# Optimization experiments

Measured on AMD Instinct MI355X. Metric: run time of the kernel, lower is better.

Reference implementation:

```python
import jax, jax.numpy as jnp
import numpy as np

B, H, W, C = 32, 56, 56, 256
K = 7  # spatial-attention conv kernel size


def setup_inputs() -> dict:
    key = jax.random.key(0)
    kx, kw = jax.random.split(key)
    x = jax.random.normal(kx, (B, H, W, C), dtype=jnp.float32)
    # he_normal init for a 7x7 conv with 2 input channels
    fan_in = K * K * 2
    conv_w = jax.random.normal(kw, (K, K, 2, 1), dtype=jnp.float32) * jnp.sqrt(2.0 / fan_in)
    return {"x": x, "conv_w": conv_w}


def reference(x, conv_w):
    # channel-wise avg and max pooling -> [B,H,W,2]
    avg_pool = jnp.mean(x, axis=-1, keepdims=True)
    max_pool = jnp.max(x, axis=-1, keepdims=True)
    concat = jnp.concatenate([avg_pool, max_pool], axis=-1)
    # 7x7 conv, 2 -> 1 channels, SAME padding, no bias, sigmoid activation
    attn = jax.lax.conv_general_dilated(
        concat, conv_w,
        window_strides=(1, 1), padding="SAME",
        dimension_numbers=("NHWC", "HWIO", "NHWC"),
    )
    attn = jax.nn.sigmoid(attn)  # [B,H,W,1]
    return x * attn
```

## Files before the change

### kernel.cpp

```cpp
#include <hip/hip_runtime.h>
#include <math.h>

#define BB 32
#define HH 56
#define WW 56
#define CC 256
#define KS 7
#define NPIX (BB * HH * WW)
#define NWPAIR (NPIX / 2)

typedef float vfloat4 __attribute__((ext_vector_type(4)));

template <int CTRL, int RM, int BM>
__device__ __forceinline__ float dpp_add(float v) {
    const int iv = __float_as_int(v);
    const int sh = __builtin_amdgcn_update_dpp(iv, iv, CTRL, RM, BM, false);
    return v + __int_as_float(sh);
}
template <int CTRL, int RM, int BM>
__device__ __forceinline__ float dpp_max(float v) {
    const int iv = __float_as_int(v);
    const int sh = __builtin_amdgcn_update_dpp(iv, iv, CTRL, RM, BM, false);
    return fmaxf(v, __int_as_float(sh));
}

__device__ __forceinline__ float wave_sum(float s) {
    s = dpp_add<0x111, 0xf, 0xf>(s);
    s = dpp_add<0x112, 0xf, 0xf>(s);
    s = dpp_add<0x114, 0xf, 0xe>(s);
    s = dpp_add<0x118, 0xf, 0xc>(s);
    s = dpp_add<0x142, 0xa, 0xf>(s);
    s = dpp_add<0x143, 0xc, 0xf>(s);
    return __int_as_float(__builtin_amdgcn_readlane(__float_as_int(s), 63));
}
__device__ __forceinline__ float wave_max(float m) {
    m = dpp_max<0x111, 0xf, 0xf>(m);
    m = dpp_max<0x112, 0xf, 0xf>(m);
    m = dpp_max<0x114, 0xf, 0xe>(m);
    m = dpp_max<0x118, 0xf, 0xc>(m);
    m = dpp_max<0x142, 0xa, 0xf>(m);
    m = dpp_max<0x143, 0xc, 0xf>(m);
    return __int_as_float(__builtin_amdgcn_readlane(__float_as_int(m), 63));
}

__global__ __launch_bounds__(256) void pool_kernel(const float* __restrict__ x,
                                                   float4* __restrict__ pooled4) {
    const int wave = threadIdx.x >> 6;
    const int lane = threadIdx.x & 63;
    const int wid = blockIdx.x * 4 + wave;

    const size_t base = (size_t)wid * 128 + lane;
    const vfloat4 v0 = reinterpret_cast<const vfloat4*>(x)[base];
    const vfloat4 v1 = reinterpret_cast<const vfloat4*>(x)[base + 64];

    float s0 = (v0.x + v0.y) + (v0.z + v0.w);
    float m0 = fmaxf(fmaxf(v0.x, v0.y), fmaxf(v0.z, v0.w));
    float s1 = (v1.x + v1.y) + (v1.z + v1.w);
    float m1 = fmaxf(fmaxf(v1.x, v1.y), fmaxf(v1.z, v1.w));

    s0 = wave_sum(s0);
    s1 = wave_sum(s1);
    m0 = wave_max(m0);
    m1 = wave_max(m1);

    if (lane == 0) {
        pooled4[wid] = make_float4(s0 * (1.0f / CC), m0, s1 * (1.0f / CC), m1);
    }
}

__global__ __launch_bounds__(256) void fused_kernel(const float* __restrict__ x,
                                                    const float2* __restrict__ pooled,
                                                    const float2* __restrict__ cwv,
                                                    float* __restrict__ out) {
    const int wave = threadIdx.x >> 6;
    const int lane = threadIdx.x & 63;
    const int wid = blockIdx.x * 4 + wave;

    const size_t base = (size_t)wid * 128 + lane;
    const vfloat4 v0 = reinterpret_cast<const vfloat4*>(x)[base];
    const vfloat4 v1 = reinterpret_cast<const vfloat4*>(x)[base + 64];

    const int pix0 = wid * 2;
    const int wcol0 = pix0 % WW;
    const int t = pix0 / WW;
    const int hrow = t % HH;
    const int b = t / HH;

    float pa = 0.0f, pb = 0.0f;
    if (lane < KS * KS) {
        const int ky = lane / KS;
        const int kx = lane - ky * KS;
        const int yy = hrow + ky - 3;
        if (yy >= 0 && yy < HH) {
            const float2* __restrict__ row = pooled + ((size_t)b * HH + yy) * WW;
            const float2 w = cwv[lane];
            const int xx0 = wcol0 + kx - 3;
            const int xx1 = xx0 + 1;
            if (xx0 >= 0 && xx0 < WW) {
                const float2 p = row[xx0];
                pa = fmaf(p.x, w.x, p.y * w.y);
            }
            if (xx1 >= 0 && xx1 < WW) {
                const float2 p = row[xx1];
                pb = fmaf(p.x, w.x, p.y * w.y);
            }
        }
    }
    pa = wave_sum(pa);
    pb = wave_sum(pb);
    const float att0 = 1.0f / (1.0f + expf(-pa));
    const float att1 = 1.0f / (1.0f + expf(-pb));

    reinterpret_cast<vfloat4*>(out)[base]      = v0 * att0;
    reinterpret_cast<vfloat4*>(out)[base + 64] = v1 * att1;
}

extern "C" void kernel_launch(void* const* d_in, const int* in_sizes, int n_in,
                              void* d_out, int out_size, void* d_ws, size_t ws_size,
                              hipStream_t stream) {
    const float* x = (const float*)d_in[0];
    const float2* cw = (const float2*)d_in[1];
    float* out = (float*)d_out;
    float2* pooled = (float2*)d_ws;

    const int grid = NWPAIR / 4;
    pool_kernel<<<grid, 256, 0, stream>>>(x, (float4*)pooled);
    fused_kernel<<<grid, 256, 0, stream>>>(x, pooled, cw, out);
}
```

Measured before the change: 51.26 us.

## Fuse pooling and attention into one cooperative kernel with register-resident x

Replaces the two-kernel pipeline with a single cooperative kernel. Each wave loads 49 pixels of x into registers, computes the channel avg/max pools, synchronizes the whole grid, then runs the 7x7 conv and sigmoid and writes the scaled output from those registers. This removes the second read of x from global memory and one kernel launch. In exchange it needs 196 VGPRs per lane for the cached data, so occupancy is low. It also pays for a grid-wide barrier, and the per-pixel loads and pooled writes become serialized with little latency hiding.

After: 51.42 us. Within noise of the previous version (+0.3%).

```diff
diff --git a/kernel.cpp b/kernel.cpp
--- a/kernel.cpp
+++ b/kernel.cpp
@@ -1,4 +1,5 @@
 #include <hip/hip_runtime.h>
+#include <hip/hip_cooperative_groups.h>
 #include <math.h>
 
 #define BB 32
@@ -7,9 +8,17 @@
 #define CC 256
 #define KS 7
 #define NPIX (BB * HH * WW)
+
+#define NBLK 256
+#define TPB 512
+#define WPB 8
+#define PXW 49
+
 #define NWPAIR (NPIX / 2)
 
 typedef float vfloat4 __attribute__((ext_vector_type(4)));
+
+namespace cg = cooperative_groups;
 
 template <int CTRL, int RM, int BM>
 __device__ __forceinline__ float dpp_add(float v) {
@@ -23,7 +32,6 @@
     const int sh = __builtin_amdgcn_update_dpp(iv, iv, CTRL, RM, BM, false);
     return fmaxf(v, __int_as_float(sh));
 }
-
 __device__ __forceinline__ float wave_sum(float s) {
     s = dpp_add<0x111, 0xf, 0xf>(s);
     s = dpp_add<0x112, 0xf, 0xf>(s);
@@ -41,6 +49,72 @@
     m = dpp_max<0x142, 0xa, 0xf>(m);
     m = dpp_max<0x143, 0xc, 0xf>(m);
     return __int_as_float(__builtin_amdgcn_readlane(__float_as_int(m), 63));
+}
+
+__global__ __launch_bounds__(TPB, 2) void spatial_attn_all(
+    const float* __restrict__ x,
+    float2* __restrict__ pooled,
+    const float2* __restrict__ cwv,
+    float* __restrict__ out)
+{
+    const int wave = threadIdx.x >> 6;
+    const int lane = threadIdx.x & 63;
+    const int wid = blockIdx.x * WPB + wave;
+
+    const vfloat4* __restrict__ x4 = reinterpret_cast<const vfloat4*>(x);
+    const size_t base = (size_t)wid * (PXW * 64) + lane;
+
+    vfloat4 a[PXW];
+#pragma unroll
+    for (int p = 0; p < PXW; ++p) {
+        a[p] = x4[base + (size_t)p * 64];
+    }
+
+    const int pix0 = wid * PXW;
+#pragma unroll
+    for (int p = 0; p < PXW; ++p) {
+        float s = (a[p].x + a[p].y) + (a[p].z + a[p].w);
+        float m = fmaxf(fmaxf(a[p].x, a[p].y), fmaxf(a[p].z, a[p].w));
+        s = wave_sum(s);
+        m = wave_max(m);
+        if (lane == 0) {
+            pooled[pix0 + p] = make_float2(s * (1.0f / CC), m);
+        }
+    }
+
+    cg::this_grid().sync();
+
+    const bool active = lane < KS * KS;
+    int ky = 0, kx = 0;
+    float2 wgt = make_float2(0.0f, 0.0f);
+    if (active) {
+        ky = lane / KS;
+        kx = lane - ky * KS;
+        wgt = cwv[lane];
+    }
+
+#pragma unroll
+    for (int p = 0; p < PXW; ++p) {
+        const int pix = pix0 + p;
+        const int wcol = pix % WW;
+        const int t = pix / WW;
+        const int hrow = t % HH;
+        const int bimg = t / HH;
+
+        float pa = 0.0f;
+        if (active) {
+            const int yy = hrow + ky - 3;
+            const int xx = wcol + kx - 3;
+            if ((unsigned)yy < HH && (unsigned)xx < WW) {
+                const float2 pv = pooled[((size_t)bimg * HH + yy) * WW + xx];
+                pa = fmaf(pv.x, wgt.x, pv.y * wgt.y);
+            }
+        }
+        pa = wave_sum(pa);
+        const float att = 1.0f / (1.0f + expf(-pa));
+
+        reinterpret_cast<vfloat4*>(out)[base + (size_t)p * 64] = a[p] * att;
+    }
 }
 
 __global__ __launch_bounds__(256) void pool_kernel(const float* __restrict__ x,
@@ -123,7 +197,17 @@
     float* out = (float*)d_out;
     float2* pooled = (float2*)d_ws;
 
-    const int grid = NWPAIR / 4;
-    pool_kernel<<<grid, 256, 0, stream>>>(x, (float4*)pooled);
-    fused_kernel<<<grid, 256, 0, stream>>>(x, pooled, cw, out);
-}
+    int maxb = 0;
+    hipError_t oe = hipOccupancyMaxActiveBlocksPerMultiprocessor(
+        &maxb, (const void*)spatial_attn_all, TPB, 0);
+
+    if (oe == hipSuccess && maxb >= 1) {
+        void* args[] = {(void*)&x, (void*)&pooled, (void*)&cw, (void*)&out};
+        hipLaunchCooperativeKernel((void*)spatial_attn_all, dim3(NBLK), dim3(TPB),
+                                   args, 0, stream);
+    } else {
+        const int grid = NWPAIR / 4;
+        pool_kernel<<<grid, 256, 0, stream>>>(x, (float4*)pooled);
+        fused_kernel<<<grid, 256, 0, stream>>>(x, pooled, cw, out);
+    }
+}
```
